# Performance work log

Measured on AMD Instinct MI355X. Metric: run time of the kernel, lower is better.

## Reference

```python
import math
import jax, jax.numpy as jnp
from jax import lax
import numpy as np

STRIDES = (8, 16, 32)            # p3, p4, p5
ANCHOR_STRIDE_SCALE = 8
ASPECT_RATIOS = (0.5, 1.0, 2.0)  # A = 3
NMS_THRESH = 0.6
PRE_NMS_TOPK = 400
POST_NMS_TOPK = 50
BBOX_CLAMP = 4.135166556742356   # log(1000/16)


def setup_inputs() -> dict:
    key = jax.random.key(0)
    ks = jax.random.split(key, 8)
    C = 256
    inp = {
        "p3": jax.random.normal(ks[0], (8, C, 128, 128), jnp.float32),
        "p4": jax.random.normal(ks[1], (8, C, 64, 64), jnp.float32),
        "p5": jax.random.normal(ks[2], (8, C, 32, 32), jnp.float32),
        # fan-in scaled weights so logits/deltas stay in a sane range
        "w_stem": jax.random.normal(ks[3], (C, C, 3, 3), jnp.float32) * (1.0 / math.sqrt(C * 9)),
        "b_stem": jnp.zeros((C,), jnp.float32),
        "w_obj": jax.random.normal(ks[4], (3, C, 1, 1), jnp.float32) * (1.0 / math.sqrt(C)),
        "b_obj": jnp.zeros((3,), jnp.float32),
        "w_box": jax.random.normal(ks[5], (12, C, 1, 1), jnp.float32) * (0.01 / math.sqrt(C)),
        "b_box": jnp.zeros((12,), jnp.float32),
    }
    return inp


def _conv(x, w, b, pad):
    y = lax.conv_general_dilated(x, w, (1, 1), pad,
                                 dimension_numbers=("NCHW", "OIHW", "NCHW"))
    return y + b[None, :, None, None]


def _make_anchors(H, W, stride):
    # anchor centers at (x+0.5)*stride ; base size = stride * anchor_stride_scale
    xs = (jnp.arange(W, dtype=jnp.float32) + 0.5) * stride
    ys = (jnp.arange(H, dtype=jnp.float32) + 0.5) * stride
    cx, cy = jnp.meshgrid(xs, ys)              # (H, W), row-major matches H*W flatten
    cx = cx.reshape(-1)
    cy = cy.reshape(-1)
    size = float(stride * ANCHOR_STRIDE_SCALE)
    per_ratio = []
    for r in ASPECT_RATIOS:
        w = size / math.sqrt(r)
        h = size * math.sqrt(r)
        per_ratio.append(jnp.stack([cx - w / 2, cy - h / 2, cx + w / 2, cy + h / 2], axis=-1))
    return jnp.stack(per_ratio, axis=1).reshape(-1, 4)  # (H*W*A, 4)


def _decode(deltas, anchors):
    aw = anchors[:, 2] - anchors[:, 0]
    ah = anchors[:, 3] - anchors[:, 1]
    acx = anchors[:, 0] + 0.5 * aw
    acy = anchors[:, 1] + 0.5 * ah
    dx, dy = deltas[:, 0], deltas[:, 1]
    dw = jnp.clip(deltas[:, 2], -BBOX_CLAMP, BBOX_CLAMP)
    dh = jnp.clip(deltas[:, 3], -BBOX_CLAMP, BBOX_CLAMP)
    pcx = acx + dx * aw
    pcy = acy + dy * ah
    pw = aw * jnp.exp(dw)
    ph = ah * jnp.exp(dh)
    return jnp.stack([pcx - 0.5 * pw, pcy - 0.5 * ph,
                      pcx + 0.5 * pw, pcy + 0.5 * ph], axis=-1)


def _nms_keep(boxes, thresh):
    # boxes already sorted by descending score; greedy class-agnostic NMS
    N = boxes.shape[0]
    x1, y1, x2, y2 = boxes[:, 0], boxes[:, 1], boxes[:, 2], boxes[:, 3]
    area = jnp.maximum(x2 - x1, 0.0) * jnp.maximum(y2 - y1, 0.0)
    ix1 = jnp.maximum(x1[:, None], x1[None, :])
    iy1 = jnp.maximum(y1[:, None], y1[None, :])
    ix2 = jnp.minimum(x2[:, None], x2[None, :])
    iy2 = jnp.minimum(y2[:, None], y2[None, :])
    inter = jnp.maximum(ix2 - ix1, 0.0) * jnp.maximum(iy2 - iy1, 0.0)
    iou = inter / jnp.maximum(area[:, None] + area[None, :] - inter, 1e-8)  # (N, N)
    idx = jnp.arange(N)

    def body(keep, i):
        suppress = (iou[i] > thresh) & keep[i] & (idx > i)
        return keep & ~suppress, 0

    keep, _ = lax.scan(body, jnp.ones((N,), bool), idx)
    return keep


def _proposals_one_image(logits, deltas, anchors):
    # logits: (N,), deltas: (N, 4), anchors: (N, 4)
    k = min(PRE_NMS_TOPK, logits.shape[0])
    scores, top_idx = lax.top_k(logits, k)
    boxes = _decode(deltas[top_idx], anchors[top_idx])
    keep = _nms_keep(boxes, NMS_THRESH)
    masked = jnp.where(keep, scores, -jnp.inf)
    _, kidx = lax.top_k(masked, POST_NMS_TOPK)
    return boxes[kidx]  # (POST_NMS_TOPK, 4)


def _rpn_level(feat, w_stem, b_stem, w_obj, b_obj, w_box, b_box, stride):
    B, _, H, W = feat.shape
    x = jax.nn.relu(_conv(feat, w_stem, b_stem, "SAME"))       # stem: 3x3 conv + ReLU
    obj = _conv(x, w_obj, b_obj, "VALID")                      # (B, A, H, W)
    box = _conv(x, w_box, b_box, "VALID")                      # (B, 4A, H, W)
    A = obj.shape[1]
    obj = obj.transpose(0, 2, 3, 1).reshape(B, H * W * A)       # (B, HWA)
    box = box.transpose(0, 2, 3, 1).reshape(B, H * W * A, 4)    # (B, HWA, 4)
    anchors = _make_anchors(H, W, stride)                       # (HWA, 4)
    return jax.vmap(lambda o, d: _proposals_one_image(o, d, anchors))(obj, box)


def reference(p3, p4, p5, w_stem, b_stem, w_obj, b_obj, w_box, b_box):
    out = []
    for feat, stride in zip((p3, p4, p5), STRIDES):
        out.append(_rpn_level(feat, w_stem, b_stem, w_obj, b_obj, w_box, b_box, stride))
    # (B, 3 * POST_NMS_TOPK, 4) absolute XYXY proposals, concatenated across levels
    return jnp.concatenate(out, axis=1)
```

## Files before the change

### kernel.cpp

```cpp
#include <hip/hip_runtime.h>
#include <math.h>
#include <stdint.h>

#define BBOX_CLAMP 4.135166556742356f
#define SQH 0.70710678118654752f
#define SQ2 1.41421356237309515f

typedef __attribute__((ext_vector_type(8))) short s8b;
typedef __attribute__((ext_vector_type(4))) float f32x4;
typedef __attribute__((ext_vector_type(4))) short s4b;

__device__ __forceinline__ unsigned okey(float f){
  unsigned u = __float_as_uint(f);
  return (u & 0x80000000u) ? ~u : (u | 0x80000000u);
}
__device__ __forceinline__ unsigned short f2bf(float f){
  unsigned u = __float_as_uint(f);
  unsigned r = (u + 0x7FFFu + ((u >> 16) & 1u)) >> 16;
  return (unsigned short)r;
}
__device__ __forceinline__ float bf2f(unsigned short h){
  return __uint_as_float(((unsigned)h) << 16);
}

__global__ void k_wsplit(const float* __restrict__ w,
                         unsigned short* __restrict__ whi, unsigned short* __restrict__ wlo){
  const int ck = blockIdx.x;
  const int cout = threadIdx.x;
  const int cin = ck / 9, tap = ck - cin*9;
  const float x = w[cout*2304 + ck];
  const unsigned short h = f2bf(x);
  const unsigned short lo2 = f2bf(x - bf2f(h));
  const int slice = cin >> 5, g = (cin >> 3) & 3, j = cin & 7;
  const size_t off = ((((size_t)tap*8 + slice)*4 + g)*256 + cout)*8 + j;
  whi[off] = h; wlo[off] = lo2;
}

__global__ __launch_bounds__(256, 2) void k_stem_mfma(
    const float* __restrict__ p3f, const float* __restrict__ p4f, const float* __restrict__ p5f,
    const unsigned short* __restrict__ whi, const unsigned short* __restrict__ wlo,
    const float* __restrict__ bstem,
    const float* __restrict__ wobj, const float* __restrict__ bobj,
    const float* __restrict__ wbox, const float* __restrict__ bbox,
    float* __restrict__ sc3, float* __restrict__ dl3,
    float* __restrict__ sc4, float* __restrict__ dl4,
    float* __restrict__ sc5, float* __restrict__ dl5)
{
  __shared__ __align__(16) unsigned char smem[34816];
  unsigned short* Abuf = reinterpret_cast<unsigned short*>(smem);
  float* part = reinterpret_cast<float*>(smem);

  const int tid = threadIdx.x;
  const int l = tid & 63, w = tid >> 6;
  const int li = l & 15, g = l >> 4;

  int id = blockIdx.x;
  const float* feat; float* scores; float* deltas; int H, W, bx, by, b;
  if (id < 1024){ feat=p3f; scores=sc3; deltas=dl3; H=128; W=128;
      bx = id & 3; by = (id >> 2) & 31; b = id >> 7; }
  else if (id < 1280){ id -= 1024; feat=p4f; scores=sc4; deltas=dl4; H=64; W=64;
      bx = id & 1; by = (id >> 1) & 15; b = id >> 5; }
  else { id -= 1280; feat=p5f; scores=sc5; deltas=dl5; H=32; W=32;
      bx = 0; by = id & 7; b = id >> 3; }
  const int px0 = bx*32, py0 = by*4;
  const size_t HW = (size_t)H*W;
  const float* fb = feat + (size_t)b*256*HW;

  const int gr = tid / 34, gc = tid - gr*34;
  const int row = py0 + gr - 1, col = px0 + gc - 1;
  const bool inb = (tid < 204) && row >= 0 && row < H && col >= 0 && col < W;
  const bool lact = (tid < 204);
  const float* gA = fb + ((size_t)(inb ? row : 0)*W + (inb ? col : 0));

  f32x4 acc[8][4];
#pragma unroll
  for (int m=0;m<8;++m)
#pragma unroll
    for (int cg=0;cg<4;++cg) acc[m][cg] = (f32x4){0.f,0.f,0.f,0.f};

  const int lig = li*40 + g*8;

  for (int slice = 0; slice < 8; ++slice){
    __syncthreads();
    const float* gs = gA + (size_t)slice*32*HW;
#pragma unroll
    for (int ch = 0; ch < 8; ++ch){
      float x0=0.f, x1=0.f, x2=0.f, x3=0.f;
      if (inb){
        x0 = gs[(size_t)(ch*4+0)*HW];
        x1 = gs[(size_t)(ch*4+1)*HW];
        x2 = gs[(size_t)(ch*4+2)*HW];
        x3 = gs[(size_t)(ch*4+3)*HW];
      }
      if (lact){
        const unsigned short h0=f2bf(x0), h1=f2bf(x1), h2=f2bf(x2), h3=f2bf(x3);
        s4b hv; hv[0]=(short)h0; hv[1]=(short)h1; hv[2]=(short)h2; hv[3]=(short)h3;
        s4b lv; lv[0]=(short)f2bf(x0-bf2f(h0)); lv[1]=(short)f2bf(x1-bf2f(h1));
                lv[2]=(short)f2bf(x2-bf2f(h2)); lv[3]=(short)f2bf(x3-bf2f(h3));
        *reinterpret_cast<s4b*>(&Abuf[tid*40 + ch*4]) = hv;
        *reinterpret_cast<s4b*>(&Abuf[8160 + tid*40 + ch*4]) = lv;
      }
    }
    __syncthreads();

    for (int tap = 0; tap < 9; ++tap){
      const int dr = tap/3 - 1, dc = tap - (tap/3)*3 - 1;
      s8b bh[4], bl[4];
#pragma unroll
      for (int cg = 0; cg < 4; ++cg){
        const int woff = ((((tap*8 + slice)*4 + g)*256) + (w*64 + cg*16 + li))*8;
        bh[cg] = *reinterpret_cast<const s8b*>(&whi[woff]);
        bl[cg] = *reinterpret_cast<const s8b*>(&wlo[woff]);
      }
      const int tb = (dr*34 + dc)*40;
#pragma unroll
      for (int m = 0; m < 8; ++m){
        const int rm = m >> 1, cm = m & 1;
        const int aoff = ((rm+1)*34 + cm*16 + 1)*40 + lig + tb;
        const s8b ahi = *reinterpret_cast<const s8b*>(&Abuf[aoff]);
        const s8b alo = *reinterpret_cast<const s8b*>(&Abuf[8160 + aoff]);
#pragma unroll
        for (int cg = 0; cg < 4; ++cg){
          acc[m][cg] = __builtin_amdgcn_mfma_f32_16x16x32_bf16(ahi, bh[cg], acc[m][cg], 0, 0, 0);
          acc[m][cg] = __builtin_amdgcn_mfma_f32_16x16x32_bf16(ahi, bl[cg], acc[m][cg], 0, 0, 0);
          acc[m][cg] = __builtin_amdgcn_mfma_f32_16x16x32_bf16(alo, bh[cg], acc[m][cg], 0, 0, 0);
        }
      }
    }
  }

#pragma unroll
  for (int cg = 0; cg < 4; ++cg){
    const float bsv = bstem[w*64 + cg*16 + li];
#pragma unroll
    for (int m = 0; m < 8; ++m)
#pragma unroll
      for (int r = 0; r < 4; ++r)
        acc[m][cg][r] = fmaxf(acc[m][cg][r] + bsv, 0.f);
  }

  __syncthreads();

#pragma unroll
  for (int oc = 0; oc < 15; ++oc){
    float wv[4];
#pragma unroll
    for (int cg = 0; cg < 4; ++cg){
      const int cc = w*64 + cg*16 + li;
      wv[cg] = (oc < 3) ? wobj[oc*256 + cc] : wbox[(oc-3)*256 + cc];
    }
#pragma unroll
    for (int m = 0; m < 8; ++m){
#pragma unroll
      for (int r = 0; r < 4; ++r){
        float t = acc[m][0][r] * wv[0];
        t = fmaf(acc[m][1][r], wv[1], t);
        t = fmaf(acc[m][2][r], wv[2], t);
        t = fmaf(acc[m][3][r], wv[3], t);
        t += __shfl_xor(t, 1, 64);
        t += __shfl_xor(t, 2, 64);
        t += __shfl_xor(t, 4, 64);
        t += __shfl_xor(t, 8, 64);
        if (li == 0){
          const int rm = m >> 1, cm = m & 1;
          const int px = rm*32 + cm*16 + g*4 + r;
          part[(w*128 + px)*17 + oc] = t;
        }
      }
    }
  }
  __syncthreads();

  {
    const int px = tid & 127, half = tid >> 7;
    const int rm2 = px >> 5, rem = px & 31;
    const int hh = py0 + rm2, ww = px0 + rem;
    const size_t loc = (size_t)hh*W + ww;
    const int oce = half ? 15 : 8;
    for (int oc = half*8; oc < oce; ++oc){
      float s = ((part[(0*128+px)*17+oc] + part[(1*128+px)*17+oc])
               +  part[(2*128+px)*17+oc]) + part[(3*128+px)*17+oc];
      s += (oc < 3) ? bobj[oc] : bbox[oc-3];
      if (oc < 3) scores[(size_t)b*HW*3 + loc*3 + oc] = s;
      else        deltas[(size_t)b*HW*12 + loc*12 + (oc-3)] = s;
    }
  }
}

__global__ __launch_bounds__(1024) void k_select(
    const float* __restrict__ sc3, const float* __restrict__ sc4, const float* __restrict__ sc5,
    const float* __restrict__ dl3, const float* __restrict__ dl4, const float* __restrict__ dl5,
    float* __restrict__ out)
{
  const int lvl = blockIdx.x >> 3;
  const int b   = blockIdx.x & 7;
  int N, W; float stride; const float* sc; const float* dl;
  if (lvl==0){ N=49152; W=128; stride=8.f;  sc=sc3; dl=dl3; }
  else if (lvl==1){ N=12288; W=64; stride=16.f; sc=sc4; dl=dl4; }
  else { N=3072; W=32; stride=32.f; sc=sc5; dl=dl5; }
  sc += (size_t)b*N;
  dl += (size_t)b*(size_t)(N/3)*12;

  __shared__ unsigned hist[256];
  __shared__ unsigned s_prefix;
  __shared__ int s_need;
  __shared__ int s_cntc;
  __shared__ unsigned long long cand[1024];
  __shared__ int tk[400];
  __shared__ float bx1[400], by1[400], bx2[400], by2[400], bar_[400];
  __shared__ unsigned long long mask[400][7];
  __shared__ int olist[50];

  const int t = threadIdx.x;

  if (t==0){ s_prefix=0u; s_need=400; }
  for (int pass=0; pass<4; ++pass){
    const int shift = 24 - 8*pass;
    if (t<256) hist[t]=0u;
    __syncthreads();
    const unsigned pref = s_prefix;
    for (int i=t; i<N; i+=1024){
      const unsigned k = okey(sc[i]);
      if (pass==0 || (k >> (shift+8)) == pref)
        atomicAdd(&hist[(k>>shift)&255u], 1u);
    }
    __syncthreads();
    if (t==0){
      int need = s_need, cum=0, bsel=0;
      for (int bb=255; bb>=0; --bb){
        const int h = (int)hist[bb];
        if (cum + h >= need){ bsel=bb; break; }
        cum += h;
      }
      s_prefix = (pref<<8) | (unsigned)bsel;
      s_need = need - cum;
    }
    __syncthreads();
  }
  const unsigned K = s_prefix;

  if (t==0) s_cntc = 0;
  cand[t] = 0ull;
  __syncthreads();
  for (int i=t; i<N; i+=1024){
    const unsigned k = okey(sc[i]);
    if (k >= K){
      const int pos = atomicAdd(&s_cntc, 1);
      if (pos < 1024)
        cand[pos] = ((unsigned long long)k<<32) | (unsigned long long)(0xFFFFFFFFu - (unsigned)i);
    }
  }
  __syncthreads();

  for (int kk=2; kk<=1024; kk<<=1){
    for (int j=kk>>1; j>0; j>>=1){
      const int ixj = t ^ j;
      if (ixj > t){
        const unsigned long long a = cand[t], c = cand[ixj];
        const bool descending = ((t & kk) == 0);
        if ((a < c) == descending){ cand[t]=c; cand[ixj]=a; }
      }
      __syncthreads();
    }
  }

  if (t < 400){
    const unsigned long long c = cand[t];
    const int gi = (int)(0xFFFFFFFFu - (unsigned)(c & 0xFFFFFFFFull));
    tk[t] = gi;
    const int loc = gi/3, a = gi - loc*3;
    const int hh = loc / W, ww = loc - hh*W;
    const float cx = (ww + 0.5f)*stride, cy = (hh + 0.5f)*stride;
    const float size = stride*8.f;
    const float sq = (a==0) ? SQH : ((a==1) ? 1.f : SQ2);
    const float hw_ = 0.5f*(size/sq);
    const float hv_ = 0.5f*(size*sq);
    const float ax1 = cx - hw_, ax2 = cx + hw_;
    const float ay1 = cy - hv_, ay2 = cy + hv_;
    const float aw = ax2 - ax1, ah = ay2 - ay1;
    const float acx = ax1 + 0.5f*aw, acy = ay1 + 0.5f*ah;
    const float* dd = dl + (size_t)loc*12 + a*4;
    const float dx = dd[0], dy = dd[1];
    const float dw = fminf(fmaxf(dd[2], -BBOX_CLAMP), BBOX_CLAMP);
    const float dh = fminf(fmaxf(dd[3], -BBOX_CLAMP), BBOX_CLAMP);
    const float pcx = acx + dx*aw;
    const float pcy = acy + dy*ah;
    const float pw = aw*expf(dw);
    const float ph = ah*expf(dh);
    const float x1 = pcx - 0.5f*pw, y1 = pcy - 0.5f*ph;
    const float x2 = pcx + 0.5f*pw, y2 = pcy + 0.5f*ph;
    bx1[t]=x1; by1[t]=y1; bx2[t]=x2; by2[t]=y2;
    bar_[t] = fmaxf(x2-x1, 0.f)*fmaxf(y2-y1, 0.f);
  }
  __syncthreads();

  for (int task=t; task<2800; task+=1024){
    const int i = task/7, w = task - (task/7)*7;
    unsigned long long m = 0ull;
    const float xi1=bx1[i], yi1=by1[i], xi2=bx2[i], yi2=by2[i], ai=bar_[i];
    const int j0 = w<<6;
    const int js = (j0 > i+1) ? j0 : (i+1);
    const int je = (j0+64 < 400) ? (j0+64) : 400;
    for (int j=js; j<je; ++j){
      const float ix1 = fmaxf(xi1, bx1[j]);
      const float iy1 = fmaxf(yi1, by1[j]);
      const float ix2 = fminf(xi2, bx2[j]);
      const float iy2 = fminf(yi2, by2[j]);
      const float inter = fmaxf(ix2-ix1, 0.f)*fmaxf(iy2-iy1, 0.f);
      const float iou = inter / fmaxf(ai + bar_[j] - inter, 1e-8f);
      if (iou > 0.6f) m |= (1ull << (j - j0));
    }
    mask[i][w] = m;
  }
  __syncthreads();

  if (t==0){
    unsigned long long keepw[7];
#pragma unroll
    for (int w=0;w<7;++w) keepw[w] = ~0ull;
    for (int i=0;i<400;++i){
      if ((keepw[i>>6] >> (i&63)) & 1ull){
#pragma unroll
        for (int w=0;w<7;++w) keepw[w] &= ~mask[i][w];
      }
    }
    int cnt=0;
    for (int i=0;i<400 && cnt<50;++i) if ( (keepw[i>>6]>>(i&63)) & 1ull) olist[cnt++]=i;
    for (int i=0;i<400 && cnt<50;++i) if (!((keepw[i>>6]>>(i&63)) & 1ull)) olist[cnt++]=i;
  }
  __syncthreads();

  if (t < 50){
    const int j = olist[t];
    float* o = out + (size_t)b*600 + (size_t)(lvl*50 + t)*4;
    o[0]=bx1[j]; o[1]=by1[j]; o[2]=bx2[j]; o[3]=by2[j];
  }
}

extern "C" void kernel_launch(void* const* d_in, const int* in_sizes, int n_in,
                              void* d_out, int out_size, void* d_ws, size_t ws_size,
                              hipStream_t stream) {
  (void)in_sizes; (void)n_in; (void)out_size; (void)ws_size;
  const float* p3     = (const float*)d_in[0];
  const float* p4     = (const float*)d_in[1];
  const float* p5     = (const float*)d_in[2];
  const float* w_stem = (const float*)d_in[3];
  const float* b_stem = (const float*)d_in[4];
  const float* w_obj  = (const float*)d_in[5];
  const float* b_obj  = (const float*)d_in[6];
  const float* w_box  = (const float*)d_in[7];
  const float* b_box  = (const float*)d_in[8];
  float* out = (float*)d_out;

  unsigned short* whi = (unsigned short*)d_ws;
  unsigned short* wlo = whi + 589824;
  float* sc3 = (float*)(wlo + 589824);
  float* sc4 = sc3 + 393216;
  float* sc5 = sc4 + 98304;
  float* dl3 = sc5 + 24576;
  float* dl4 = dl3 + 1572864;
  float* dl5 = dl4 + 393216;

  k_wsplit<<<dim3(2304), dim3(256), 0, stream>>>(w_stem, whi, wlo);

  k_stem_mfma<<<dim3(1344), dim3(256), 0, stream>>>(
      p3, p4, p5, whi, wlo, b_stem, w_obj, b_obj, w_box, b_box,
      sc3, dl3, sc4, dl4, sc5, dl5);

  k_select<<<dim3(24), dim3(1024), 0, stream>>>(sc3, sc4, sc5, dl3, dl4, dl5, out);
}
```

Measured before the change: 832.5 us.

## Re-tile stem MFMA waves as 2x2 pixel-by-cout grid to cut LDS reads

Changes the per-wave tile of the 3x3 stem conv. Each wave used to cover all 128 pixels against 64 output channels; it now covers 64 pixels (two rows) against 128 output channels. This halves the A-fragment LDS reads per tap and doubles reuse of each A fragment, at the cost of twice as many weight-fragment loads from global/L2. The head epilogue now sums two partials per pixel instead of four, and shared memory shrinks to just the A buffer size.

```diff
diff --git a/kernel.cpp b/kernel.cpp
--- a/kernel.cpp
+++ b/kernel.cpp
@@ -46,13 +46,14 @@
     float* __restrict__ sc4, float* __restrict__ dl4,
     float* __restrict__ sc5, float* __restrict__ dl5)
 {
-  __shared__ __align__(16) unsigned char smem[34816];
+  __shared__ __align__(16) unsigned char smem[32640];
   unsigned short* Abuf = reinterpret_cast<unsigned short*>(smem);
   float* part = reinterpret_cast<float*>(smem);
 
   const int tid = threadIdx.x;
   const int l = tid & 63, w = tid >> 6;
   const int li = l & 15, g = l >> 4;
+  const int p = w >> 1, c = w & 1;
 
   int id = blockIdx.x;
   const float* feat; float* scores; float* deltas; int H, W, bx, by, b;
@@ -72,13 +73,11 @@
   const bool lact = (tid < 204);
   const float* gA = fb + ((size_t)(inb ? row : 0)*W + (inb ? col : 0));
 
-  f32x4 acc[8][4];
-#pragma unroll
-  for (int m=0;m<8;++m)
-#pragma unroll
-    for (int cg=0;cg<4;++cg) acc[m][cg] = (f32x4){0.f,0.f,0.f,0.f};
-
-  const int lig = li*40 + g*8;
+  f32x4 acc[4][8];
+#pragma unroll
+  for (int m=0;m<4;++m)
+#pragma unroll
+    for (int cg=0;cg<8;++cg) acc[m][cg] = (f32x4){0.f,0.f,0.f,0.f};
 
   for (int slice = 0; slice < 8; ++slice){
     __syncthreads();
@@ -105,35 +104,45 @@
 
     for (int tap = 0; tap < 9; ++tap){
       const int dr = tap/3 - 1, dc = tap - (tap/3)*3 - 1;
-      s8b bh[4], bl[4];
-#pragma unroll
-      for (int cg = 0; cg < 4; ++cg){
-        const int woff = ((((tap*8 + slice)*4 + g)*256) + (w*64 + cg*16 + li))*8;
-        bh[cg] = *reinterpret_cast<const s8b*>(&whi[woff]);
-        bl[cg] = *reinterpret_cast<const s8b*>(&wlo[woff]);
-      }
-      const int tb = (dr*34 + dc)*40;
-#pragma unroll
-      for (int m = 0; m < 8; ++m){
-        const int rm = m >> 1, cm = m & 1;
-        const int aoff = ((rm+1)*34 + cm*16 + 1)*40 + lig + tb;
-        const s8b ahi = *reinterpret_cast<const s8b*>(&Abuf[aoff]);
-        const s8b alo = *reinterpret_cast<const s8b*>(&Abuf[8160 + aoff]);
-#pragma unroll
-        for (int cg = 0; cg < 4; ++cg){
-          acc[m][cg] = __builtin_amdgcn_mfma_f32_16x16x32_bf16(ahi, bh[cg], acc[m][cg], 0, 0, 0);
-          acc[m][cg] = __builtin_amdgcn_mfma_f32_16x16x32_bf16(ahi, bl[cg], acc[m][cg], 0, 0, 0);
-          acc[m][cg] = __builtin_amdgcn_mfma_f32_16x16x32_bf16(alo, bh[cg], acc[m][cg], 0, 0, 0);
+      s8b ah[4], al[4];
+#pragma unroll
+      for (int m = 0; m < 4; ++m){
+        const int rm = 2*p + (m >> 1), cm = m & 1;
+        const int aoff = ((rm+dr+1)*34 + cm*16 + li + dc + 1)*40 + g*8;
+        ah[m] = *reinterpret_cast<const s8b*>(&Abuf[aoff]);
+        al[m] = *reinterpret_cast<const s8b*>(&Abuf[8160 + aoff]);
+      }
+#pragma unroll
+      for (int chunk = 0; chunk < 2; ++chunk){
+        s8b bh[4], bl[4];
+#pragma unroll
+        for (int cg4 = 0; cg4 < 4; ++cg4){
+          const int cout = c*128 + (chunk*4 + cg4)*16 + li;
+          const int woff = ((((tap*8 + slice)*4 + g)*256) + cout)*8;
+          bh[cg4] = *reinterpret_cast<const s8b*>(&whi[woff]);
+          bl[cg4] = *reinterpret_cast<const s8b*>(&wlo[woff]);
         }
-      }
-    }
-  }
-
-#pragma unroll
-  for (int cg = 0; cg < 4; ++cg){
-    const float bsv = bstem[w*64 + cg*16 + li];
-#pragma unroll
-    for (int m = 0; m < 8; ++m)
+#pragma unroll
+        for (int m = 0; m < 4; ++m){
+#pragma unroll
+          for (int cg4 = 0; cg4 < 4; ++cg4)
+            acc[m][chunk*4+cg4] = __builtin_amdgcn_mfma_f32_16x16x32_bf16(ah[m], bh[cg4], acc[m][chunk*4+cg4], 0, 0, 0);
+#pragma unroll
+          for (int cg4 = 0; cg4 < 4; ++cg4)
+            acc[m][chunk*4+cg4] = __builtin_amdgcn_mfma_f32_16x16x32_bf16(ah[m], bl[cg4], acc[m][chunk*4+cg4], 0, 0, 0);
+#pragma unroll
+          for (int cg4 = 0; cg4 < 4; ++cg4)
+            acc[m][chunk*4+cg4] = __builtin_amdgcn_mfma_f32_16x16x32_bf16(al[m], bh[cg4], acc[m][chunk*4+cg4], 0, 0, 0);
+        }
+      }
+    }
+  }
+
+#pragma unroll
+  for (int cg = 0; cg < 8; ++cg){
+    const float bsv = bstem[c*128 + cg*16 + li];
+#pragma unroll
+    for (int m = 0; m < 4; ++m)
 #pragma unroll
       for (int r = 0; r < 4; ++r)
         acc[m][cg][r] = fmaxf(acc[m][cg][r] + bsv, 0.f);
@@ -143,43 +152,41 @@
 
 #pragma unroll
   for (int oc = 0; oc < 15; ++oc){
-    float wv[4];
-#pragma unroll
-    for (int cg = 0; cg < 4; ++cg){
-      const int cc = w*64 + cg*16 + li;
+    float wv[8];
+#pragma unroll
+    for (int cg = 0; cg < 8; ++cg){
+      const int cc = c*128 + cg*16 + li;
       wv[cg] = (oc < 3) ? wobj[oc*256 + cc] : wbox[(oc-3)*256 + cc];
     }
 #pragma unroll
-    for (int m = 0; m < 8; ++m){
+    for (int m = 0; m < 4; ++m){
 #pragma unroll
       for (int r = 0; r < 4; ++r){
         float t = acc[m][0][r] * wv[0];
-        t = fmaf(acc[m][1][r], wv[1], t);
-        t = fmaf(acc[m][2][r], wv[2], t);
-        t = fmaf(acc[m][3][r], wv[3], t);
+#pragma unroll
+        for (int cg = 1; cg < 8; ++cg) t = fmaf(acc[m][cg][r], wv[cg], t);
         t += __shfl_xor(t, 1, 64);
         t += __shfl_xor(t, 2, 64);
         t += __shfl_xor(t, 4, 64);
         t += __shfl_xor(t, 8, 64);
-        if (li == 0){
-          const int rm = m >> 1, cm = m & 1;
-          const int px = rm*32 + cm*16 + g*4 + r;
-          part[(w*128 + px)*17 + oc] = t;
-        }
+        if (li == 0)
+          part[(w*64 + m*16 + g*4 + r)*17 + oc] = t;
       }
     }
   }
   __syncthreads();
 
   {
-    const int px = tid & 127, half = tid >> 7;
-    const int rm2 = px >> 5, rem = px & 31;
-    const int hh = py0 + rm2, ww = px0 + rem;
+    const int p_idx = tid & 127, half = tid >> 7;
+    const int mg = p_idx >> 4, i16 = p_idx & 15;
+    const int rm = mg >> 1, cm = mg & 1;
+    const int pp = mg >> 2, ml = mg & 3;
+    const int hh = py0 + rm, ww = px0 + cm*16 + i16;
     const size_t loc = (size_t)hh*W + ww;
     const int oce = half ? 15 : 8;
     for (int oc = half*8; oc < oce; ++oc){
-      float s = ((part[(0*128+px)*17+oc] + part[(1*128+px)*17+oc])
-               +  part[(2*128+px)*17+oc]) + part[(3*128+px)*17+oc];
+      float s = part[((2*pp)*64 + ml*16 + i16)*17 + oc]
+              + part[((2*pp+1)*64 + ml*16 + i16)*17 + oc];
       s += (oc < 3) ? bobj[oc] : bbox[oc-3];
       if (oc < 3) scores[(size_t)b*HW*3 + loc*3 + oc] = s;
       else        deltas[(size_t)b*HW*12 + loc*12 + (oc-3)] = s;
```

Result: faster. 790.7 us (-5.0%).
